# Optimization experiments

Hardware: AMD Instinct MI355X
Metric: run time of the kernel (lower is better)

## Reference

```python
import jax, jax.numpy as jnp
import numpy as np

B, N, D = 8, 1024, 768
H = 3
DCAT = 2 * D          # 1536, input dim at layer 1
DK = DCAT // H        # 512
CONV_OUT = D - 2      # 766 (kernel 3, VALID)


def setup_inputs() -> dict:
    key = jax.random.key(0)
    ks = jax.random.split(key, 20)
    s = 0.02
    return {
        "adj": jax.random.uniform(ks[0], (B, N, N), dtype=jnp.float32),
        "inputs": jax.random.normal(ks[1], (B, N, D), dtype=jnp.float32),
        "score_mask": jax.random.randint(ks[2], (B, H, N, N), 0, 2).astype(bool),
        # GCN layer weights (stored [in,out]; math = torch Linear)
        "W0_w": jax.random.normal(ks[3], (D, D), dtype=jnp.float32) * s,
        "W0_b": jnp.zeros((D,), dtype=jnp.float32),
        "W1_w": jax.random.normal(ks[4], (DCAT, D), dtype=jnp.float32) * s,
        "W1_b": jnp.zeros((D,), dtype=jnp.float32),
        # MultiHeadAttention(3, 1536) query/key projections
        "q_w": jax.random.normal(ks[5], (DCAT, DCAT), dtype=jnp.float32) * s,
        "q_b": jnp.zeros((DCAT,), dtype=jnp.float32),
        "k_w": jax.random.normal(ks[6], (DCAT, DCAT), dtype=jnp.float32) * s,
        "k_b": jnp.zeros((DCAT,), dtype=jnp.float32),
        # Conv1d(n, n, 3) created in forward: OIH layout
        "conv_w": jax.random.normal(ks[7], (N, N, 3), dtype=jnp.float32) * s,
        "conv_b": jnp.zeros((N,), dtype=jnp.float32),
        # linearc: 766 -> 768
        "linc_w": jax.random.normal(ks[8], (CONV_OUT, D), dtype=jnp.float32) * s,
        "linc_b": jnp.zeros((D,), dtype=jnp.float32),
        # fc: Linear(768,768,no bias) -> ReLU -> Linear(768,768,no bias)
        "fc1_w": jax.random.normal(ks[9], (D, D), dtype=jnp.float32) * s,
        "fc2_w": jax.random.normal(ks[10], (D, D), dtype=jnp.float32) * s,
    }


def _gcn_layer(adj, x, denom, Ww, Wb):
    Ax = adj @ x                       # [B,n,din]
    AxW = (Ax @ Ww + Wb) / denom       # [B,n,768]
    return jax.nn.relu(AxW) + (x @ Ww + Wb)


def _select_top2(m):
    # per-batch top-2 threshold over flattened NxN, symmetrize, diag=1
    b, n, _ = m.shape
    flat = m.reshape(b, -1)
    thr = jax.lax.top_k(flat, 2)[0][:, -1]                  # [b]
    mask = (flat >= thr[:, None]).astype(m.dtype).reshape(b, n, n)
    mask = mask + jnp.swapaxes(mask, -1, -2)
    eye = jnp.eye(n, dtype=m.dtype)
    return mask * (1.0 - eye) + eye


def reference(adj, inputs, score_mask, W0_w, W0_b, W1_w, W1_b,
              q_w, q_b, k_w, k_b, conv_w, conv_b, linc_w, linc_b,
              fc1_w, fc2_w):
    b, n, d = inputs.shape
    # ---- layer 0 ----
    denom = adj.sum(2, keepdims=True) + 1.0
    out = _gcn_layer(adj, inputs, denom, W0_w, W0_b)        # [B,n,768]
    # Conv1d over feature axis with channels = n, VALID, k=3 -> [B,n,766]
    conve = jax.nn.relu(
        jax.lax.conv_general_dilated(out, conv_w, (1,), 'VALID',
                                     dimension_numbers=('NCH', 'OIH', 'NCH'))
        + conv_b[None, :, None])
    out = conve @ linc_w + linc_b                           # [B,n,768]
    # ---- layer 1 (semantic path) ----
    x = jnp.concatenate([inputs, out], axis=-1)             # [B,n,1536]
    h, dk = H, x.shape[-1] // H
    q = (x @ q_w + q_b).reshape(b, n, h, dk).transpose(0, 2, 1, 3)
    k = (x @ k_w + k_b).reshape(b, n, h, dk).transpose(0, 2, 1, 3)
    scores = jnp.einsum('bhqd,bhkd->bhqk', q, k) / jnp.sqrt(jnp.float32(dk))
    scores = jnp.where(score_mask, jnp.float32(-1e9), scores)
    keep = (~score_mask[:, :, :, 0:1]).astype(scores.dtype)
    attn = jax.nn.softmax(scores, axis=-1) * keep           # [B,3,n,n]
    # attention-driven head selection (softmax over batch dim, argmax over heads)
    prob = jax.nn.softmax(attn.sum((-2, -1)), axis=0)       # [B,3]
    max_idx = jnp.argmax(prob, axis=1)                      # [B]
    adj2 = jnp.take_along_axis(attn, max_idx[:, None, None, None], axis=1)[:, 0]
    adj2 = _select_top2(adj2) * adj2
    denom2 = adj2.sum(2, keepdims=True) + 1.0
    out = _gcn_layer(adj2, x, denom2, W1_w, W1_b)
    out = jax.nn.relu(out @ fc1_w) @ fc2_w
    return out
```

## Files before the change

kernel.cpp:

```cpp
#include <hip/hip_runtime.h>
#include <cstdint>
#include <cstddef>

typedef __bf16 bf16;
typedef __bf16 bf16x8 __attribute__((ext_vector_type(8)));
typedef float f32x4 __attribute__((ext_vector_type(4)));

#define B_ 8
#define N_ 1024
#define D_ 768
#define H_ 3
#define DC_ 1536
#define DK_ 512
#define PC_ 766
#define MB_ (1024ull*1024ull)

static const size_t O_DEN   = 0;
static const size_t O_DEN2  = 32768;
static const size_t O_ADIAG = 65536;
static const size_t O_T2P   = 98304;
static const size_t O_THR   = 163840;
static const size_t O_CNTS  = 164096;
static const size_t O_HSEL  = 164352;
static const size_t O_SELC  = 164608;
static const size_t O_FLAG  = 164864;
static const size_t O_QKB   = 165120;
static const size_t O_SEL   = 180224;
static const size_t O_ATTN  = 262144;
static const size_t O_X     = O_ATTN + 32*MB_;
static const size_t O_AX2   = O_X    + 24*MB_;
static const size_t O_ADJB  = O_AX2  + 24*MB_;
static const size_t O_INT   = O_ADJB + 16*MB_;
static const size_t O_BBA   = O_INT  + 12*MB_;
static const size_t O_BBB   = O_BBA  + 12*MB_;
static const size_t O_BBC   = O_BBB  + 12*MB_;
static const size_t O_W0T   = O_BBC  + 12*MB_;
static const size_t O_W1T   = O_W0T + 1179648;
static const size_t O_QKWT  = O_W1T + 2359296;
static const size_t O_CWB   = O_QKWT + 9437184;
static const size_t O_LCT   = O_CWB + 6291456;
static const size_t O_F1T   = O_LCT + 1179648;
static const size_t O_F2T   = O_F1T + 1179648;
static const size_t WS_NEED = O_F2T + 1179648;
static const size_t O_OUT0T = O_INT;

__device__ __forceinline__ bool mask_at(const void* p, int flag, size_t i) {
    switch (flag) {
        case 1:  return ((const int*)p)[i] != 0;
        case 2:  return ((const float*)p)[i] != 0.0f;
        case 3:  return ((const long long*)p)[i] != 0;
        default: return ((const unsigned char*)p)[i] != 0;
    }
}

__device__ __forceinline__ void gload16(const void* g, void* l) {
    __builtin_amdgcn_global_load_lds(
        (const __attribute__((address_space(1))) void*)g,
        (__attribute__((address_space(3))) void*)l, 16, 0, 0);
}

__device__ inline float blockMax256(float v) {
    __shared__ float red[4];
    for (int off = 32; off; off >>= 1) v = fmaxf(v, __shfl_xor(v, off));
    int lane = threadIdx.x & 63, wid = threadIdx.x >> 6;
    if (lane == 0) red[wid] = v;
    __syncthreads();
    v = fmaxf(fmaxf(red[0], red[1]), fmaxf(red[2], red[3]));
    __syncthreads();
    return v;
}

__device__ inline float blockSum256(float v) {
    __shared__ float red[4];
    for (int off = 32; off; off >>= 1) v += __shfl_xor(v, off);
    int lane = threadIdx.x & 63, wid = threadIdx.x >> 6;
    if (lane == 0) red[wid] = v;
    __syncthreads();
    v = red[0] + red[1] + red[2] + red[3];
    __syncthreads();
    return v;
}

template<int EPI>
__global__ __launch_bounds__(256) void mm(
    const bf16* __restrict__ A, size_t sA, int lda,
    const bf16* __restrict__ Bt, size_t sB, int ldb,
    const int* __restrict__ rowIdx, int rowMul,
    const float* __restrict__ bias,
    const bf16* __restrict__ Dadd, int ldd,
    const float* __restrict__ denv,
    const void* __restrict__ smask, const int* __restrict__ flagp,
    bf16* __restrict__ Cb, float* __restrict__ Cf, size_t sC, int ldc,
    int M, int N, int K)
{
    __shared__ __align__(16) bf16 As[2][64 * 64];
    __shared__ __align__(16) bf16 Bs[2][128 * 64];

    const int gx = gridDim.x, gy = gridDim.y;
    const int nwg = gx * gy * (int)gridDim.z;
    int lin = ((int)blockIdx.z * gy + (int)blockIdx.y) * gx + (int)blockIdx.x;
    int cpx = nwg >> 3;
    int swz = (lin & 7) * cpx + (lin >> 3);
    int ty = swz % gy;
    int tt = swz / gy;
    int tx = tt % gx;
    int b  = tt / gx;

    const int bm = ty * 64, bn = tx * 128;
    const int tid = threadIdx.x;
    const int lane = tid & 63, w = tid >> 6;
    const int wr = w >> 1, wc = w & 1;
    const int boff = rowIdx ? rowIdx[b] * rowMul : 0;

    const bf16* Ab = A + (size_t)b * sA;
    const bf16* Bb = Bt + (size_t)b * sB;

    const int sr = lane >> 3;
    const int gk = ((lane & 7) ^ (lane >> 3)) * 8;

    f32x4 zero = {0.f, 0.f, 0.f, 0.f};
    f32x4 acc[2][4];
    #pragma unroll
    for (int i = 0; i < 2; ++i)
        #pragma unroll
        for (int j = 0; j < 4; ++j) acc[i][j] = zero;

    #pragma unroll
    for (int q = 0; q < 2; ++q)
        gload16((const void*)(Ab + (size_t)(bm + w * 16 + q * 8 + sr) * lda + gk),
                (void*)(As[0] + (w * 16 + q * 8) * 64));
    #pragma unroll
    for (int q = 0; q < 4; ++q)
        gload16((const void*)(Bb + (size_t)(boff + bn + w * 32 + q * 8 + sr) * ldb + gk),
                (void*)(Bs[0] + (w * 32 + q * 8) * 64));

    const int rl = lane & 15;
    const int g8 = lane >> 4;
    const int rx = lane & 7;

    int cur = 0;
    for (int k0 = 0; k0 < K; k0 += 64) {
        int nxt = cur ^ 1;
        if (k0 + 64 < K) {
            #pragma unroll
            for (int q = 0; q < 2; ++q)
                gload16((const void*)(Ab + (size_t)(bm + w * 16 + q * 8 + sr) * lda + k0 + 64 + gk),
                        (void*)(As[nxt] + (w * 16 + q * 8) * 64));
            #pragma unroll
            for (int q = 0; q < 4; ++q)
                gload16((const void*)(Bb + (size_t)(boff + bn + w * 32 + q * 8 + sr) * ldb + k0 + 64 + gk),
                        (void*)(Bs[nxt] + (w * 32 + q * 8) * 64));
            asm volatile("s_waitcnt vmcnt(6)" ::: "memory");
        } else {
            asm volatile("s_waitcnt vmcnt(0)" ::: "memory");
        }
        __builtin_amdgcn_s_barrier();
        __builtin_amdgcn_sched_barrier(0);

        bf16x8 af[2][2], bfv[4][2];
        #pragma unroll
        for (int ks = 0; ks < 2; ++ks) {
            int e = ks * 4 + g8;
            #pragma unroll
            for (int i = 0; i < 2; ++i)
                af[i][ks] = *(const bf16x8*)(As[cur] + (wr * 32 + i * 16 + rl) * 64 + (e ^ rx) * 8);
            #pragma unroll
            for (int j = 0; j < 4; ++j)
                bfv[j][ks] = *(const bf16x8*)(Bs[cur] + (wc * 64 + j * 16 + rl) * 64 + (e ^ rx) * 8);
        }
        #pragma unroll
        for (int ks = 0; ks < 2; ++ks)
            #pragma unroll
            for (int i = 0; i < 2; ++i)
                #pragma unroll
                for (int j = 0; j < 4; ++j)
                    acc[i][j] = __builtin_amdgcn_mfma_f32_16x16x32_bf16(af[i][ks], bfv[j][ks], acc[i][j], 0, 0, 0);

        __builtin_amdgcn_s_barrier();
        __builtin_amdgcn_sched_barrier(0);
        cur = nxt;
    }

    const int r0 = (lane >> 4) * 4, c0 = lane & 15;
    int flag = 0, h0 = 0;
    if (EPI == 4) { flag = flagp[0]; h0 = rowIdx[b]; }
    #pragma unroll
    for (int i = 0; i < 2; ++i) {
        #pragma unroll
        for (int r = 0; r < 4; ++r) {
            int m = bm + wr * 32 + i * 16 + r0 + r;
            #pragma unroll
            for (int j = 0; j < 4; ++j) {
                int n = bn + wc * 64 + j * 16 + c0;
                float v = acc[i][j][r];
                size_t oidx = (size_t)b * sC + (size_t)m * ldc + n;
                if (EPI == 0) {
                    Cb[oidx] = (bf16)(v + bias[boff + n]);
                } else if (EPI == 1) {
                    v = fmaxf((v + bias[n]) / denv[(size_t)b * M + m], 0.f)
                        + (float)Dadd[((size_t)b * M + m) * ldd + n];
                    Cb[oidx] = (bf16)v;
                } else if (EPI == 2) {
                    Cb[oidx] = (bf16)fmaxf(v, 0.f);
                } else if (EPI == 3) {
                    Cf[oidx] = v;
                } else if (EPI == 4) {
                    size_t mi = (((size_t)b * H_ + h0) * N_ + m) * N_ + n;
                    Cf[oidx] = mask_at(smask, flag, mi) ? -1e9f : v * 0.04419417382415922f;
                } else if (EPI == 5) {
                    Cb[oidx] = (n < PC_) ? (bf16)fmaxf(v + bias[m], 0.f) : (bf16)0.f;
                } else {
                    Cb[oidx] = (bf16)v;
                }
            }
        }
    }
}


__global__ __launch_bounds__(256) void k_detect(const unsigned int* __restrict__ sm,
                                                int* __restrict__ flag) {
    __shared__ int sGt1, sF32, sOddNZ;
    if (threadIdx.x == 0) { sGt1 = 0; sF32 = 0; sOddNZ = 0; }
    __syncthreads();
    int gt1 = 0, f32c = 0, oddnz = 0;
    for (int s = 0; s < 16; ++s) {
        int idx = s * 256 + threadIdx.x;
        unsigned wv = sm[idx];
        if (wv > 1u) gt1 = 1;
        if (wv == 0x3F800000u) f32c++;
        if ((idx & 1) && wv != 0u) oddnz = 1;
    }
    if (gt1)   atomicOr(&sGt1, 1);
    if (f32c)  atomicAdd(&sF32, f32c);
    if (oddnz) atomicOr(&sOddNZ, 1);
    __syncthreads();
    if (threadIdx.x == 0) {
        int f;
        if (sF32 > 512) f = 2;
        else if (!sGt1) f = sOddNZ ? 1 : 3;
        else f = 0;
        flag[0] = f;
    }
}

__global__ __launch_bounds__(256) void k_cvt_adj(const float* __restrict__ adj,
                                                 bf16* __restrict__ adjb,
                                                 float* __restrict__ den) {
    int b = blockIdx.y, row = blockIdx.x;
    size_t base = ((size_t)b * N_ + row) * N_;
    float4 v = ((const float4*)(adj + base))[threadIdx.x];
    union { bf16 b[4]; uint2 u; } o;
    o.b[0] = (bf16)v.x; o.b[1] = (bf16)v.y; o.b[2] = (bf16)v.z; o.b[3] = (bf16)v.w;
    ((uint2*)(adjb + base))[threadIdx.x] = o.u;
    float s = blockSum256(v.x + v.y + v.z + v.w);
    if (threadIdx.x == 0) den[b * N_ + row] = s + 1.0f;
}

__global__ __launch_bounds__(256) void k_cvtrows(const float* __restrict__ s,
                                                 bf16* __restrict__ d) {
    int row = blockIdx.x, t = threadIdx.x;
    if (t >= 192) return;
    float4 v = ((const float4*)(s + (size_t)row * D_))[t];
    union { bf16 b[4]; uint2 u; } o;
    o.b[0] = (bf16)v.x; o.b[1] = (bf16)v.y; o.b[2] = (bf16)v.z; o.b[3] = (bf16)v.w;
    *(uint2*)(d + (size_t)row * DC_ + t * 4) = o.u;
}

__global__ __launch_bounds__(256) void k_cw2(const float* __restrict__ w,
                                             bf16* __restrict__ d) {
    int o = blockIdx.x;
    const float* s = w + (size_t)o * 3072;
    bf16* dp = d + (size_t)o * 3072;
    for (int q = 0; q < 4; ++q) {
        int i = q * 256 + threadIdx.x;
        float v0 = s[i * 3], v1 = s[i * 3 + 1], v2 = s[i * 3 + 2];
        dp[i] = (bf16)v0; dp[1024 + i] = (bf16)v1; dp[2048 + i] = (bf16)v2;
    }
}

__global__ __launch_bounds__(256) void k_qkb(const float* __restrict__ qb,
                                             const float* __restrict__ kb,
                                             float* __restrict__ d) {
    int idx = blockIdx.x * 256 + threadIdx.x;
    if (idx >= 3072) return;
    int h = idx >> 10, rem = idx & 1023, s = rem >> 9, r = rem & 511;
    d[idx] = (s ? kb : qb)[h * 512 + r];
}

__global__ __launch_bounds__(256) void k_trcvt(
    const float* __restrict__ src, bf16* __restrict__ dst,
    int R, int C, int Rpad, int Cpad, size_t sSrc, size_t sDst, int mode)
{
    __shared__ float t[32][33];
    int b = blockIdx.z;
    int r0 = blockIdx.y * 32, c0 = blockIdx.x * 32;
    int tx = threadIdx.x & 31, ty = threadIdx.x >> 5;
    const float* s = src + (size_t)b * sSrc;
    bf16* d = dst + (size_t)b * sDst;
    #pragma unroll
    for (int q = 0; q < 4; ++q) {
        int r = r0 + ty + q * 8, c = c0 + tx;
        t[ty + q * 8][tx] = (r < R && c < C) ? s[(size_t)r * C + c] : 0.f;
    }
    __syncthreads();
    #pragma unroll
    for (int q = 0; q < 4; ++q) {
        int dr = c0 + ty + q * 8, dc = r0 + tx;
        if (dr < Cpad && dc < Rpad) {
            int drm = dr;
            if (mode == 1) drm = (dr >> 9) * 1024 + (dr & 511);
            else if (mode == 2) drm = (dr >> 9) * 1024 + 512 + (dr & 511);
            d[(size_t)drm * Rpad + dc] = (bf16)t[tx][ty + q * 8];
        }
    }
}

__global__ __launch_bounds__(256) void k_tr_bf16(const bf16* __restrict__ src,
                                                 bf16* __restrict__ dst) {
    __shared__ bf16 t[32][34];
    int b = blockIdx.z;
    int i0 = blockIdx.y * 32, p0 = blockIdx.x * 32;
    int tx = threadIdx.x & 31, ty = threadIdx.x >> 5;
    const bf16* s = src + (size_t)b * N_ * D_;
    bf16* d = dst + (size_t)b * D_ * N_;
    #pragma unroll
    for (int q = 0; q < 4; ++q)
        t[ty + q * 8][tx] = s[(size_t)(i0 + ty + q * 8) * D_ + p0 + tx];
    __syncthreads();
    #pragma unroll
    for (int q = 0; q < 4; ++q)
        d[(size_t)(p0 + ty + q * 8) * N_ + i0 + tx] = t[tx][ty + q * 8];
}

__global__ __launch_bounds__(256) void k_softmax(float* __restrict__ Sc,
                                                 const void* __restrict__ smask,
                                                 const int* __restrict__ flagp,
                                                 const int* __restrict__ hsel,
                                                 float* __restrict__ part) {
    __shared__ float s1[256], s2[256];
    int b = blockIdx.y, row = blockIdx.x;
    int h0 = hsel[b], flag = flagp[0];
    float* rp = Sc + ((size_t)b * N_ + row) * N_;
    float v[4];
    float mx = -INFINITY;
    #pragma unroll
    for (int s = 0; s < 4; ++s) { v[s] = rp[s * 256 + threadIdx.x]; mx = fmaxf(mx, v[s]); }
    mx = blockMax256(mx);
    float sum = 0.f;
    #pragma unroll
    for (int s = 0; s < 4; ++s) { v[s] = expf(v[s] - mx); sum += v[s]; }
    sum = blockSum256(sum);
    size_t ki = (((size_t)b * H_ + h0) * N_ + row) * N_;
    float keep = mask_at(smask, flag, ki) ? 0.f : 1.f;
    float inv = keep / sum;
    float m1 = -INFINITY, m2 = -INFINITY;
    #pragma unroll
    for (int s = 0; s < 4; ++s) {
        float x = v[s] * inv;
        rp[s * 256 + threadIdx.x] = x;
        if (x > m1) { m2 = m1; m1 = x; } else m2 = fmaxf(m2, x);
    }
    int tid = threadIdx.x;
    s1[tid] = m1; s2[tid] = m2;
    __syncthreads();
    for (int off = 128; off; off >>= 1) {
        if (tid < off) {
            float a1 = s1[tid], a2 = s2[tid], b1 = s1[tid + off], b2 = s2[tid + off];
            s1[tid] = fmaxf(a1, b1);
            s2[tid] = fmaxf(fminf(a1, b1), fmaxf(a2, b2));
        }
        __syncthreads();
    }
    if (tid == 0) {
        part[((size_t)b * N_ + row) * 2]     = s1[0];
        part[((size_t)b * N_ + row) * 2 + 1] = s2[0];
    }
}

__global__ __launch_bounds__(256) void k_count(const void* __restrict__ smask,
                                               const int* __restrict__ flagp,
                                               int* __restrict__ counts) {
    int bh = blockIdx.x, flag = flagp[0];
    float c = 0.f;
    for (int s = 0; s < 4; ++s) {
        int q = s * 256 + threadIdx.x;
        size_t mi = ((size_t)bh * N_ + q) * N_;
        if (!mask_at(smask, flag, mi)) c += 1.f;
    }
    c = blockSum256(c);
    if (threadIdx.x == 0) counts[bh] = (int)(c + 0.5f);
}

__global__ void k_select_head(const int* __restrict__ counts, int* __restrict__ hsel) {
    if (threadIdx.x != 0 || blockIdx.x != 0) return;
    float p[B_][H_];
    for (int h = 0; h < H_; ++h) {
        float mx = -1e30f;
        for (int b = 0; b < B_; ++b) mx = fmaxf(mx, (float)counts[b * H_ + h]);
        float s = 0.f;
        for (int b = 0; b < B_; ++b) { p[b][h] = expf((float)counts[b * H_ + h] - mx); s += p[b][h]; }
        for (int b = 0; b < B_; ++b) p[b][h] /= s;
    }
    for (int b = 0; b < B_; ++b) {
        int best = 0; float bv = p[b][0];
        for (int h = 1; h < H_; ++h) if (p[b][h] > bv) { bv = p[b][h]; best = h; }
        hsel[b] = best;
    }
}

__global__ __launch_bounds__(256) void k_top2_s2(const float* __restrict__ part,
                                                 float* __restrict__ thr,
                                                 int* __restrict__ selcnt) {
    __shared__ float s1[256], s2[256];
    int b = blockIdx.x, tid = threadIdx.x;
    float m1 = -INFINITY, m2 = -INFINITY;
    for (int s = 0; s < 4; ++s) {
        int r = s * 256 + tid;
        float a1 = part[((size_t)b * N_ + r) * 2];
        float a2 = part[((size_t)b * N_ + r) * 2 + 1];
        float n1 = fmaxf(m1, a1);
        float n2 = fmaxf(fminf(m1, a1), fmaxf(m2, a2));
        m1 = n1; m2 = n2;
    }
    s1[tid] = m1; s2[tid] = m2;
    __syncthreads();
    for (int off = 128; off; off >>= 1) {
        if (tid < off) {
            float a1 = s1[tid], a2 = s2[tid], b1 = s1[tid + off], b2 = s2[tid + off];
            s1[tid] = fmaxf(a1, b1);
            s2[tid] = fmaxf(fminf(a1, b1), fmaxf(a2, b2));
        }
        __syncthreads();
    }
    if (tid == 0) { thr[b] = s2[0]; selcnt[b] = 0; }
}

__global__ __launch_bounds__(256) void k_extract(const float* __restrict__ attn,
                                                 const float* __restrict__ thr,
                                                 int* __restrict__ selcnt,
                                                 int* __restrict__ sel,
                                                 float* __restrict__ adiag,
                                                 float* __restrict__ den2) {
    int b = blockIdx.y, row = blockIdx.x;
    const float* ap = attn + (size_t)b * N_ * N_;
    float t = thr[b];
    size_t base = (size_t)row * 1024;
    for (int s = 0; s < 4; ++s) {
        int col = s * 256 + threadIdx.x;
        float v = ap[base + col];
        if (col == row) {
            adiag[b * N_ + row] = v;
            den2[b * N_ + row] = v + 1.0f;
        }
        if (v >= t) {
            int pos = atomicAdd(&selcnt[b], 1);
            if (pos < 512) {
                sel[((size_t)b * 512 + pos) * 2]     = row;
                sel[((size_t)b * 512 + pos) * 2 + 1] = col;
            }
        }
    }
}

__global__ __launch_bounds__(256) void k_ax2_init(const bf16* __restrict__ x,
                                                  const float* __restrict__ adiag,
                                                  bf16* __restrict__ ax2) {
    int row = blockIdx.x;
    float a = adiag[row];
    const bf16* xp = x + (size_t)row * DC_;
    bf16* op = ax2 + (size_t)row * DC_;
    for (int s = 0; s < 6; ++s) {
        int d = s * 256 + threadIdx.x;
        op[d] = (bf16)(a * (float)xp[d]);
    }
}

__global__ __launch_bounds__(256) void k_ax2_sparse(const float* __restrict__ attn,
                                                    const bf16* __restrict__ x,
                                                    const int* __restrict__ selcnt,
                                                    const int* __restrict__ sel,
                                                    bf16* __restrict__ ax2,
                                                    float* __restrict__ den2) {
    int b = blockIdx.x;
    int cnt = selcnt[b]; if (cnt > 512) cnt = 512;
    __shared__ int si[1024];
    if (threadIdx.x == 0) {
        for (int e = 0; e < cnt; ++e) {
            si[e * 2]     = sel[((size_t)b * 512 + e) * 2];
            si[e * 2 + 1] = sel[((size_t)b * 512 + e) * 2 + 1];
        }
        for (int a = 1; a < cnt; ++a) {
            int ii = si[a * 2], jj = si[a * 2 + 1];
            long long key = (long long)ii * N_ + jj;
            int p = a - 1;
            while (p >= 0 && ((long long)si[p * 2] * N_ + si[p * 2 + 1]) > key) {
                si[(p + 1) * 2] = si[p * 2]; si[(p + 1) * 2 + 1] = si[p * 2 + 1]; --p;
            }
            si[(p + 1) * 2] = ii; si[(p + 1) * 2 + 1] = jj;
        }
    }
    __syncthreads();
    const float* ap = attn + (size_t)b * N_ * N_;
    for (int e = 0; e < cnt; ++e) {
        int i = si[e * 2], j = si[e * 2 + 1];
        if (i == j) continue;
        float aij = ap[(size_t)i * N_ + j];
        float aji = ap[(size_t)j * N_ + i];
        bf16* ri = ax2 + ((size_t)b * N_ + i) * DC_;
        bf16* rj = ax2 + ((size_t)b * N_ + j) * DC_;
        const bf16* xi = x + ((size_t)b * N_ + i) * DC_;
        const bf16* xj = x + ((size_t)b * N_ + j) * DC_;
        for (int s = 0; s < 6; ++s) {
            int d = s * 256 + threadIdx.x;
            ri[d] = (bf16)((float)ri[d] + aij * (float)xj[d]);
            rj[d] = (bf16)((float)rj[d] + aji * (float)xi[d]);
        }
        if (threadIdx.x == 0) {
            den2[b * N_ + i] += aij;
            den2[b * N_ + j] += aji;
        }
        __syncthreads();
    }
}

extern "C" void kernel_launch(void* const* d_in, const int* in_sizes, int n_in,
                              void* d_out, int out_size, void* d_ws, size_t ws_size,
                              hipStream_t stream) {
    if (n_in < 17) return;
    if (ws_size < WS_NEED) return;

    const float* adj    = (const float*)d_in[0];
    const float* inputs = (const float*)d_in[1];
    const void*  smask  = d_in[2];
    const float* W0w = (const float*)d_in[3];
    const float* W0b = (const float*)d_in[4];
    const float* W1w = (const float*)d_in[5];
    const float* W1b = (const float*)d_in[6];
    const float* qw  = (const float*)d_in[7];
    const float* qb  = (const float*)d_in[8];
    const float* kw  = (const float*)d_in[9];
    const float* kb  = (const float*)d_in[10];
    const float* convw = (const float*)d_in[11];
    const float* convb = (const float*)d_in[12];
    const float* lincw = (const float*)d_in[13];
    const float* lincb = (const float*)d_in[14];
    const float* fc1w  = (const float*)d_in[15];
    const float* fc2w  = (const float*)d_in[16];

    char* W = (char*)d_ws;
    float* out = (float*)d_out;

    float* den    = (float*)(W + O_DEN);
    float* den2   = (float*)(W + O_DEN2);
    float* adiag  = (float*)(W + O_ADIAG);
    float* t2p    = (float*)(W + O_T2P);
    float* thr    = (float*)(W + O_THR);
    int*   counts = (int*)(W + O_CNTS);
    int*   hsel   = (int*)(W + O_HSEL);
    int*   selcnt = (int*)(W + O_SELC);
    int*   flag   = (int*)(W + O_FLAG);
    float* qkb    = (float*)(W + O_QKB);
    int*   sel    = (int*)(W + O_SEL);
    float* ATTN   = (float*)(W + O_ATTN);
    bf16* X     = (bf16*)(W + O_X);
    bf16* AX2   = (bf16*)(W + O_AX2);
    bf16* QKOUT = (bf16*)(W + O_AX2);
    bf16* ADJB  = (bf16*)(W + O_ADJB);
    bf16* INT_  = (bf16*)(W + O_INT);
    bf16* OUT0T = (bf16*)(W + O_OUT0T);
    bf16* BBA   = (bf16*)(W + O_BBA);
    bf16* BBB   = (bf16*)(W + O_BBB);
    bf16* BBC   = (bf16*)(W + O_BBC);
    bf16* W0T   = (bf16*)(W + O_W0T);
    bf16* W1T   = (bf16*)(W + O_W1T);
    bf16* QKWT  = (bf16*)(W + O_QKWT);
    bf16* CW2   = (bf16*)(W + O_CWB);
    bf16* LCT   = (bf16*)(W + O_LCT);
    bf16* F1T   = (bf16*)(W + O_F1T);
    bf16* F2T   = (bf16*)(W + O_F2T);

    const size_t sND  = (size_t)N_ * D_;
    const size_t sNDC = (size_t)N_ * DC_;
    const size_t sNN  = (size_t)N_ * N_;

    k_detect<<<1, 256, 0, stream>>>((const unsigned int*)smask, flag);
    k_cvt_adj<<<dim3(N_, B_), 256, 0, stream>>>(adj, ADJB, den);
    k_cvtrows<<<B_ * N_, 256, 0, stream>>>(inputs, X);
    k_cw2<<<1024, 256, 0, stream>>>(convw, CW2);
    k_qkb<<<12, 256, 0, stream>>>(qb, kb, qkb);
    k_trcvt<<<dim3(24, 32, B_), 256, 0, stream>>>(inputs, INT_, N_, D_, N_, D_, sND, sND, 0);
    k_trcvt<<<dim3(24, 24, 1), 256, 0, stream>>>(W0w, W0T, D_, D_, D_, D_, 0, 0, 0);
    k_trcvt<<<dim3(24, 48, 1), 256, 0, stream>>>(W1w, W1T, DC_, D_, DC_, D_, 0, 0, 0);
    k_trcvt<<<dim3(48, 48, 1), 256, 0, stream>>>(qw, QKWT, DC_, DC_, DC_, DC_, 0, 0, 1);
    k_trcvt<<<dim3(48, 48, 1), 256, 0, stream>>>(kw, QKWT, DC_, DC_, DC_, DC_, 0, 0, 2);
    k_trcvt<<<dim3(24, 24, 1), 256, 0, stream>>>(lincw, LCT, PC_, D_, D_, D_, 0, 0, 0);
    k_trcvt<<<dim3(24, 24, 1), 256, 0, stream>>>(fc1w, F1T, D_, D_, D_, D_, 0, 0, 0);
    k_trcvt<<<dim3(24, 24, 1), 256, 0, stream>>>(fc2w, F2T, D_, D_, D_, D_, 0, 0, 0);

    mm<0><<<dim3(6, 16, B_), 256, 0, stream>>>(X, sNDC, DC_, W0T, 0, D_, nullptr, 0,
        W0b, nullptr, 0, nullptr, nullptr, nullptr, BBA, nullptr, sND, D_, N_, D_, D_);
    mm<6><<<dim3(6, 16, B_), 256, 0, stream>>>(ADJB, sNN, N_, INT_, sND, N_, nullptr, 0,
        nullptr, nullptr, 0, nullptr, nullptr, nullptr, BBB, nullptr, sND, D_, N_, D_, N_);
    mm<1><<<dim3(6, 16, B_), 256, 0, stream>>>(BBB, sND, D_, W0T, 0, D_, nullptr, 0,
        W0b, BBA, D_, den, nullptr, nullptr, BBC, nullptr, sND, D_, N_, D_, D_);
    k_tr_bf16<<<dim3(24, 32, B_), 256, 0, stream>>>(BBC, OUT0T);
    mm<5><<<dim3(6, 16, B_), 256, 0, stream>>>(CW2, 0, 3072, OUT0T, sND, N_, nullptr, 0,
        convb, nullptr, 0, nullptr, nullptr, nullptr, BBB, nullptr, sND, D_, N_, D_, 3072);
    mm<0><<<dim3(6, 16, B_), 256, 0, stream>>>(BBB, sND, D_, LCT, 0, D_, nullptr, 0,
        lincb, nullptr, 0, nullptr, nullptr, nullptr, X + D_, nullptr, sNDC, DC_, N_, D_, D_);

    k_count<<<B_ * H_, 256, 0, stream>>>(smask, flag, counts);
    k_select_head<<<1, 64, 0, stream>>>(counts, hsel);

    mm<0><<<dim3(8, 16, B_), 256, 0, stream>>>(X, sNDC, DC_, QKWT, 0, DC_, hsel, 1024,
        qkb, nullptr, 0, nullptr, nullptr, nullptr, QKOUT, nullptr, sNN, N_, N_, N_, DC_);
    mm<4><<<dim3(8, 16, B_), 256, 0, stream>>>(QKOUT, sNN, N_, QKOUT + 512, sNN, N_, hsel, 0,
        nullptr, nullptr, 0, nullptr, smask, flag, nullptr, ATTN, sNN, N_, N_, N_, DK_);
    k_softmax<<<dim3(N_, B_), 256, 0, stream>>>(ATTN, smask, flag, hsel, t2p);

    k_top2_s2<<<B_, 256, 0, stream>>>(t2p, thr, selcnt);
    k_extract<<<dim3(N_, B_), 256, 0, stream>>>(ATTN, thr, selcnt, sel, adiag, den2);
    k_ax2_init<<<B_ * N_, 256, 0, stream>>>(X, adiag, AX2);
    k_ax2_sparse<<<B_, 256, 0, stream>>>(ATTN, X, selcnt, sel, AX2, den2);

    mm<0><<<dim3(6, 16, B_), 256, 0, stream>>>(X, sNDC, DC_, W1T, 0, DC_, nullptr, 0,
        W1b, nullptr, 0, nullptr, nullptr, nullptr, BBA, nullptr, sND, D_, N_, D_, DC_);
    mm<1><<<dim3(6, 16, B_), 256, 0, stream>>>(AX2, sNDC, DC_, W1T, 0, DC_, nullptr, 0,
        W1b, BBA, D_, den2, nullptr, nullptr, BBB, nullptr, sND, D_, N_, D_, DC_);

    mm<2><<<dim3(6, 16, B_), 256, 0, stream>>>(BBB, sND, D_, F1T, 0, D_, nullptr, 0,
        nullptr, nullptr, 0, nullptr, nullptr, nullptr, BBC, nullptr, sND, D_, N_, D_, D_);
    mm<3><<<dim3(6, 16, B_), 256, 0, stream>>>(BBC, sND, D_, F2T, 0, D_, nullptr, 0,
        nullptr, nullptr, 0, nullptr, nullptr, nullptr, nullptr, out, sND, D_, N_, D_, D_);
}
```

Baseline: 436.8 us.

## Merge prep kernels into one launch and fuse QK with W1 projection GEMM

Collapses the many small preprocessing launches (detect, conversions, transposes, mask counts) into one block-dispatched prep kernel. It also computes the x@W1 GEMM inside the Q/K projection launch by widening its grid to 1792 output columns, and folds the diagonal AX2 init into k_extract. The aim is to cut launch overhead and let small kernels fill the GPU together. The mask-count blocks each redo the detection step locally, and the merged GEMM writes to two outputs through a new epilogue.

```diff
diff --git a/kernel.cpp b/kernel.cpp
--- a/kernel.cpp
+++ b/kernel.cpp
@@ -91,7 +91,9 @@
     const float* __restrict__ denv,
     const void* __restrict__ smask, const int* __restrict__ flagp,
     bf16* __restrict__ Cb, float* __restrict__ Cf, size_t sC, int ldc,
-    int M, int N, int K)
+    int M, int N, int K,
+    const bf16* __restrict__ Bt2, const float* __restrict__ bias2,
+    bf16* __restrict__ Cb2, size_t sC2, int ldc2)
 {
     __shared__ __align__(16) bf16 As[2][64 * 64];
     __shared__ __align__(16) bf16 Bs[2][128 * 64];
@@ -115,6 +117,10 @@
     const bf16* Ab = A + (size_t)b * sA;
     const bf16* Bb = Bt + (size_t)b * sB;
 
+    const bf16* Bsrc = Bb;
+    int bRow0 = boff + bn;
+    if (EPI == 7 && bn >= 1024) { Bsrc = Bt2; bRow0 = bn - 1024; }
+
     const int sr = lane >> 3;
     const int gk = ((lane & 7) ^ (lane >> 3)) * 8;
 
@@ -131,7 +137,7 @@
                 (void*)(As[0] + (w * 16 + q * 8) * 64));
     #pragma unroll
     for (int q = 0; q < 4; ++q)
-        gload16((const void*)(Bb + (size_t)(boff + bn + w * 32 + q * 8 + sr) * ldb + gk),
+        gload16((const void*)(Bsrc + (size_t)(bRow0 + w * 32 + q * 8 + sr) * ldb + gk),
                 (void*)(Bs[0] + (w * 32 + q * 8) * 64));
 
     const int rl = lane & 15;
@@ -148,7 +154,7 @@
                         (void*)(As[nxt] + (w * 16 + q * 8) * 64));
             #pragma unroll
             for (int q = 0; q < 4; ++q)
-                gload16((const void*)(Bb + (size_t)(boff + bn + w * 32 + q * 8 + sr) * ldb + k0 + 64 + gk),
+                gload16((const void*)(Bsrc + (size_t)(bRow0 + w * 32 + q * 8 + sr) * ldb + k0 + 64 + gk),
                         (void*)(Bs[nxt] + (w * 32 + q * 8) * 64));
             asm volatile("s_waitcnt vmcnt(6)" ::: "memory");
         } else {
@@ -209,6 +215,11 @@
                     Cf[oidx] = mask_at(smask, flag, mi) ? -1e9f : v * 0.04419417382415922f;
                 } else if (EPI == 5) {
                     Cb[oidx] = (n < PC_) ? (bf16)fmaxf(v + bias[m], 0.f) : (bf16)0.f;
+                } else if (EPI == 7) {
+                    if (n < 1024)
+                        Cb[(size_t)b * sC + (size_t)m * ldc + n] = (bf16)(v + bias[boff + n]);
+                    else
+                        Cb2[(size_t)b * sC2 + (size_t)m * ldc2 + (n - 1024)] = (bf16)(v + bias2[n - 1024]);
                 } else {
                     Cb[oidx] = (bf16)v;
                 }
@@ -218,9 +229,8 @@
 }
 
 
-__global__ __launch_bounds__(256) void k_detect(const unsigned int* __restrict__ sm,
-                                                int* __restrict__ flag) {
-    __shared__ int sGt1, sF32, sOddNZ;
+__device__ int d_detect(const unsigned int* __restrict__ sm) {
+    __shared__ int sGt1, sF32, sOddNZ, sFlag;
     if (threadIdx.x == 0) { sGt1 = 0; sF32 = 0; sOddNZ = 0; }
     __syncthreads();
     int gt1 = 0, f32c = 0, oddnz = 0;
@@ -240,64 +250,20 @@
         if (sF32 > 512) f = 2;
         else if (!sGt1) f = sOddNZ ? 1 : 3;
         else f = 0;
-        flag[0] = f;
-    }
-}
-
-__global__ __launch_bounds__(256) void k_cvt_adj(const float* __restrict__ adj,
-                                                 bf16* __restrict__ adjb,
-                                                 float* __restrict__ den) {
-    int b = blockIdx.y, row = blockIdx.x;
-    size_t base = ((size_t)b * N_ + row) * N_;
-    float4 v = ((const float4*)(adj + base))[threadIdx.x];
-    union { bf16 b[4]; uint2 u; } o;
-    o.b[0] = (bf16)v.x; o.b[1] = (bf16)v.y; o.b[2] = (bf16)v.z; o.b[3] = (bf16)v.w;
-    ((uint2*)(adjb + base))[threadIdx.x] = o.u;
-    float s = blockSum256(v.x + v.y + v.z + v.w);
-    if (threadIdx.x == 0) den[b * N_ + row] = s + 1.0f;
-}
-
-__global__ __launch_bounds__(256) void k_cvtrows(const float* __restrict__ s,
-                                                 bf16* __restrict__ d) {
-    int row = blockIdx.x, t = threadIdx.x;
-    if (t >= 192) return;
-    float4 v = ((const float4*)(s + (size_t)row * D_))[t];
-    union { bf16 b[4]; uint2 u; } o;
-    o.b[0] = (bf16)v.x; o.b[1] = (bf16)v.y; o.b[2] = (bf16)v.z; o.b[3] = (bf16)v.w;
-    *(uint2*)(d + (size_t)row * DC_ + t * 4) = o.u;
-}
-
-__global__ __launch_bounds__(256) void k_cw2(const float* __restrict__ w,
-                                             bf16* __restrict__ d) {
-    int o = blockIdx.x;
-    const float* s = w + (size_t)o * 3072;
-    bf16* dp = d + (size_t)o * 3072;
-    for (int q = 0; q < 4; ++q) {
-        int i = q * 256 + threadIdx.x;
-        float v0 = s[i * 3], v1 = s[i * 3 + 1], v2 = s[i * 3 + 2];
-        dp[i] = (bf16)v0; dp[1024 + i] = (bf16)v1; dp[2048 + i] = (bf16)v2;
-    }
-}
-
-__global__ __launch_bounds__(256) void k_qkb(const float* __restrict__ qb,
-                                             const float* __restrict__ kb,
-                                             float* __restrict__ d) {
-    int idx = blockIdx.x * 256 + threadIdx.x;
-    if (idx >= 3072) return;
-    int h = idx >> 10, rem = idx & 1023, s = rem >> 9, r = rem & 511;
-    d[idx] = (s ? kb : qb)[h * 512 + r];
-}
-
-__global__ __launch_bounds__(256) void k_trcvt(
-    const float* __restrict__ src, bf16* __restrict__ dst,
-    int R, int C, int Rpad, int Cpad, size_t sSrc, size_t sDst, int mode)
-{
+        sFlag = f;
+    }
+    __syncthreads();
+    return sFlag;
+}
+
+__device__ void d_trcvt(const float* __restrict__ src, bf16* __restrict__ dst,
+                        int R, int C, int Rpad, int Cpad,
+                        size_t sSrc, size_t sDst, int mode, int bx, int by, int bz) {
     __shared__ float t[32][33];
-    int b = blockIdx.z;
-    int r0 = blockIdx.y * 32, c0 = blockIdx.x * 32;
+    int r0 = by * 32, c0 = bx * 32;
     int tx = threadIdx.x & 31, ty = threadIdx.x >> 5;
-    const float* s = src + (size_t)b * sSrc;
-    bf16* d = dst + (size_t)b * sDst;
+    const float* s = src + (size_t)bz * sSrc;
+    bf16* d = dst + (size_t)bz * sDst;
     #pragma unroll
     for (int q = 0; q < 4; ++q) {
         int r = r0 + ty + q * 8, c = c0 + tx;
@@ -313,6 +279,130 @@
             else if (mode == 2) drm = (dr >> 9) * 1024 + 512 + (dr & 511);
             d[(size_t)drm * Rpad + dc] = (bf16)t[tx][ty + q * 8];
         }
+    }
+}
+
+#define PB_DET   1
+#define PB_QKB   13
+#define PB_CW2   1037
+#define PB_ADJ   9229
+#define PB_ROWS  17421
+#define PB_INT   23565
+#define PB_W0    24141
+#define PB_W1    25293
+#define PB_QW    27597
+#define PB_KW    29901
+#define PB_LC    30477
+#define PB_F1    31053
+#define PB_F2    31629
+#define PB_CNT   31653
+
+__global__ __launch_bounds__(256) void k_prep(
+    const void* __restrict__ smask, int* __restrict__ flag, int* __restrict__ counts,
+    const float* __restrict__ adj, bf16* __restrict__ adjb, float* __restrict__ den,
+    const float* __restrict__ inputs, bf16* __restrict__ X, bf16* __restrict__ INT_,
+    const float* __restrict__ convw, bf16* __restrict__ CW2,
+    const float* __restrict__ qb, const float* __restrict__ kb, float* __restrict__ qkbD,
+    const float* __restrict__ W0w, bf16* __restrict__ W0T,
+    const float* __restrict__ W1w, bf16* __restrict__ W1T,
+    const float* __restrict__ qw, const float* __restrict__ kw, bf16* __restrict__ QKWT,
+    const float* __restrict__ lincw, bf16* __restrict__ LCT,
+    const float* __restrict__ fc1w, bf16* __restrict__ F1T,
+    const float* __restrict__ fc2w, bf16* __restrict__ F2T)
+{
+    const int id = blockIdx.x;
+    const size_t sND = (size_t)N_ * D_;
+    if (id < PB_DET) {
+        int f = d_detect((const unsigned int*)smask);
+        if (threadIdx.x == 0) flag[0] = f;
+    } else if (id < PB_QKB) {
+        int idx = (id - PB_DET) * 256 + threadIdx.x;
+        if (idx < 3072) {
+            int h = idx >> 10, rem = idx & 1023, s = rem >> 9, r = rem & 511;
+            qkbD[idx] = (s ? kb : qb)[h * 512 + r];
+        }
+    } else if (id < PB_CW2) {
+        int o = id - PB_QKB;
+        const float* s = convw + (size_t)o * 3072;
+        bf16* dp = CW2 + (size_t)o * 3072;
+        for (int q = 0; q < 4; ++q) {
+            int i = q * 256 + threadIdx.x;
+            float v0 = s[i * 3], v1 = s[i * 3 + 1], v2 = s[i * 3 + 2];
+            dp[i] = (bf16)v0; dp[1024 + i] = (bf16)v1; dp[2048 + i] = (bf16)v2;
+        }
+    } else if (id < PB_ADJ) {
+        int t = id - PB_CW2;
+        int row = t & 1023, b = t >> 10;
+        size_t base = ((size_t)b * N_ + row) * N_;
+        float4 v = ((const float4*)(adj + base))[threadIdx.x];
+        union { bf16 b[4]; uint2 u; } o;
+        o.b[0] = (bf16)v.x; o.b[1] = (bf16)v.y; o.b[2] = (bf16)v.z; o.b[3] = (bf16)v.w;
+        ((uint2*)(adjb + base))[threadIdx.x] = o.u;
+        float s = blockSum256(v.x + v.y + v.z + v.w);
+        if (threadIdx.x == 0) den[b * N_ + row] = s + 1.0f;
+    } else if (id < PB_ROWS) {
+        int row = id - PB_ADJ;
+        int t = threadIdx.x;
+        if (t < 192) {
+            float4 v = ((const float4*)(inputs + (size_t)row * D_))[t];
+            union { bf16 b[4]; uint2 u; } o;
+            o.b[0] = (bf16)v.x; o.b[1] = (bf16)v.y; o.b[2] = (bf16)v.z; o.b[3] = (bf16)v.w;
+            *(uint2*)(X + (size_t)row * DC_ + t * 4) = o.u;
+        }
+    } else if (id < PB_INT) {
+        int t = id - PB_ROWS;
+        int bx = t % 24; int u = t / 24; int by = u % 32; int bz = u / 32;
+        d_trcvt(inputs, INT_, N_, D_, N_, D_, sND, sND, 0, bx, by, bz);
+    } else if (id < PB_W0) {
+        int t = id - PB_INT;
+        d_trcvt(W0w, W0T, D_, D_, D_, D_, 0, 0, 0, t % 24, t / 24, 0);
+    } else if (id < PB_W1) {
+        int t = id - PB_W0;
+        d_trcvt(W1w, W1T, DC_, D_, DC_, D_, 0, 0, 0, t % 24, t / 24, 0);
+    } else if (id < PB_QW) {
+        int t = id - PB_W1;
+        d_trcvt(qw, QKWT, DC_, DC_, DC_, DC_, 0, 0, 1, t % 48, t / 48, 0);
+    } else if (id < PB_KW) {
+        int t = id - PB_QW;
+        d_trcvt(kw, QKWT, DC_, DC_, DC_, DC_, 0, 0, 2, t % 48, t / 48, 0);
+    } else if (id < PB_LC) {
+        int t = id - PB_KW;
+        d_trcvt(lincw, LCT, PC_, D_, D_, D_, 0, 0, 0, t % 24, t / 24, 0);
+    } else if (id < PB_F1) {
+        int t = id - PB_LC;
+        d_trcvt(fc1w, F1T, D_, D_, D_, D_, 0, 0, 0, t % 24, t / 24, 0);
+    } else if (id < PB_F2) {
+        int t = id - PB_F1;
+        d_trcvt(fc2w, F2T, D_, D_, D_, D_, 0, 0, 0, t % 24, t / 24, 0);
+    } else if (id < PB_CNT) {
+        int bh = id - PB_F2;
+        int f = d_detect((const unsigned int*)smask);
+        float c = 0.f;
+        for (int s = 0; s < 4; ++s) {
+            int q = s * 256 + threadIdx.x;
+            size_t mi = ((size_t)bh * N_ + q) * N_;
+            if (!mask_at(smask, f, mi)) c += 1.f;
+        }
+        c = blockSum256(c);
+        if (threadIdx.x == 0) counts[bh] = (int)(c + 0.5f);
+    }
+}
+
+
+__global__ void k_select_head(const int* __restrict__ counts, int* __restrict__ hsel) {
+    if (threadIdx.x != 0 || blockIdx.x != 0) return;
+    float p[B_][H_];
+    for (int h = 0; h < H_; ++h) {
+        float mx = -1e30f;
+        for (int b = 0; b < B_; ++b) mx = fmaxf(mx, (float)counts[b * H_ + h]);
+        float s = 0.f;
+        for (int b = 0; b < B_; ++b) { p[b][h] = expf((float)counts[b * H_ + h] - mx); s += p[b][h]; }
+        for (int b = 0; b < B_; ++b) p[b][h] /= s;
+    }
+    for (int b = 0; b < B_; ++b) {
+        int best = 0; float bv = p[b][0];
+        for (int h = 1; h < H_; ++h) if (p[b][h] > bv) { bv = p[b][h]; best = h; }
+        hsel[b] = best;
     }
 }
 
@@ -375,37 +465,6 @@
     if (tid == 0) {
         part[((size_t)b * N_ + row) * 2]     = s1[0];
         part[((size_t)b * N_ + row) * 2 + 1] = s2[0];
-    }
-}
-
-__global__ __launch_bounds__(256) void k_count(const void* __restrict__ smask,
-                                               const int* __restrict__ flagp,
-                                               int* __restrict__ counts) {
-    int bh = blockIdx.x, flag = flagp[0];
-    float c = 0.f;
-    for (int s = 0; s < 4; ++s) {
-        int q = s * 256 + threadIdx.x;
-        size_t mi = ((size_t)bh * N_ + q) * N_;
-        if (!mask_at(smask, flag, mi)) c += 1.f;
-    }
-    c = blockSum256(c);
-    if (threadIdx.x == 0) counts[bh] = (int)(c + 0.5f);
-}
-
-__global__ void k_select_head(const int* __restrict__ counts, int* __restrict__ hsel) {
-    if (threadIdx.x != 0 || blockIdx.x != 0) return;
-    float p[B_][H_];
-    for (int h = 0; h < H_; ++h) {
-        float mx = -1e30f;
-        for (int b = 0; b < B_; ++b) mx = fmaxf(mx, (float)counts[b * H_ + h]);
-        float s = 0.f;
-        for (int b = 0; b < B_; ++b) { p[b][h] = expf((float)counts[b * H_ + h] - mx); s += p[b][h]; }
-        for (int b = 0; b < B_; ++b) p[b][h] /= s;
-    }
-    for (int b = 0; b < B_; ++b) {
-        int best = 0; float bv = p[b][0];
-        for (int h = 1; h < H_; ++h) if (p[b][h] > bv) { bv = p[b][h]; best = h; }
-        hsel[b] = best;
     }
 }
 
@@ -441,7 +500,10 @@
                                                  int* __restrict__ selcnt,
                                                  int* __restrict__ sel,
                                                  float* __restrict__ adiag,
-                                                 float* __restrict__ den2) {
+                                                 float* __restrict__ den2,
+                                                 const bf16* __restrict__ x,
+                                                 bf16* __restrict__ ax2) {
+    __shared__ float sdiag;
     int b = blockIdx.y, row = blockIdx.x;
     const float* ap = attn + (size_t)b * N_ * N_;
     float t = thr[b];
@@ -452,6 +514,7 @@
         if (col == row) {
             adiag[b * N_ + row] = v;
             den2[b * N_ + row] = v + 1.0f;
+            sdiag = v;
         }
         if (v >= t) {
             int pos = atomicAdd(&selcnt[b], 1);
@@ -461,15 +524,11 @@
             }
         }
     }
-}
-
-__global__ __launch_bounds__(256) void k_ax2_init(const bf16* __restrict__ x,
-                                                  const float* __restrict__ adiag,
-                                                  bf16* __restrict__ ax2) {
-    int row = blockIdx.x;
-    float a = adiag[row];
-    const bf16* xp = x + (size_t)row * DC_;
-    bf16* op = ax2 + (size_t)row * DC_;
+    __syncthreads();
+    float a = sdiag;
+    const bf16* xp = x + ((size_t)b * N_ + row) * DC_;
+    bf16* op = ax2 + ((size_t)b * N_ + row) * DC_;
+    #pragma unroll
     for (int s = 0; s < 6; ++s) {
         int d = s * 256 + threadIdx.x;
         op[d] = (bf16)(a * (float)xp[d]);
@@ -584,53 +643,50 @@
     const size_t sNDC = (size_t)N_ * DC_;
     const size_t sNN  = (size_t)N_ * N_;
 
-    k_detect<<<1, 256, 0, stream>>>((const unsigned int*)smask, flag);
-    k_cvt_adj<<<dim3(N_, B_), 256, 0, stream>>>(adj, ADJB, den);
-    k_cvtrows<<<B_ * N_, 256, 0, stream>>>(inputs, X);
-    k_cw2<<<1024, 256, 0, stream>>>(convw, CW2);
-    k_qkb<<<12, 256, 0, stream>>>(qb, kb, qkb);
-    k_trcvt<<<dim3(24, 32, B_), 256, 0, stream>>>(inputs, INT_, N_, D_, N_, D_, sND, sND, 0);
-    k_trcvt<<<dim3(24, 24, 1), 256, 0, stream>>>(W0w, W0T, D_, D_, D_, D_, 0, 0, 0);
-    k_trcvt<<<dim3(24, 48, 1), 256, 0, stream>>>(W1w, W1T, DC_, D_, DC_, D_, 0, 0, 0);
-    k_trcvt<<<dim3(48, 48, 1), 256, 0, stream>>>(qw, QKWT, DC_, DC_, DC_, DC_, 0, 0, 1);
-    k_trcvt<<<dim3(48, 48, 1), 256, 0, stream>>>(kw, QKWT, DC_, DC_, DC_, DC_, 0, 0, 2);
-    k_trcvt<<<dim3(24, 24, 1), 256, 0, stream>>>(lincw, LCT, PC_, D_, D_, D_, 0, 0, 0);
-    k_trcvt<<<dim3(24, 24, 1), 256, 0, stream>>>(fc1w, F1T, D_, D_, D_, D_, 0, 0, 0);
-    k_trcvt<<<dim3(24, 24, 1), 256, 0, stream>>>(fc2w, F2T, D_, D_, D_, D_, 0, 0, 0);
+    k_prep<<<PB_CNT, 256, 0, stream>>>(smask, flag, counts,
+        adj, ADJB, den, inputs, X, INT_, convw, CW2,
+        qb, kb, qkb, W0w, W0T, W1w, W1T, qw, kw, QKWT,
+        lincw, LCT, fc1w, F1T, fc2w, F2T);
+    k_select_head<<<1, 64, 0, stream>>>(counts, hsel);
 
     mm<0><<<dim3(6, 16, B_), 256, 0, stream>>>(X, sNDC, DC_, W0T, 0, D_, nullptr, 0,
-        W0b, nullptr, 0, nullptr, nullptr, nullptr, BBA, nullptr, sND, D_, N_, D_, D_);
+        W0b, nullptr, 0, nullptr, nullptr, nullptr, BBA, nullptr, sND, D_, N_, D_, D_,
+        nullptr, nullptr, nullptr, 0, 0);
     mm<6><<<dim3(6, 16, B_), 256, 0, stream>>>(ADJB, sNN, N_, INT_, sND, N_, nullptr, 0,
-        nullptr, nullptr, 0, nullptr, nullptr, nullptr, BBB, nullptr, sND, D_, N_, D_, N_);
+        nullptr, nullptr, 0, nullptr, nullptr, nullptr, BBB, nullptr, sND, D_, N_, D_, N_,
+        nullptr, nullptr, nullptr, 0, 0);
     mm<1><<<dim3(6, 16, B_), 256, 0, stream>>>(BBB, sND, D_, W0T, 0, D_, nullptr, 0,
-        W0b, BBA, D_, den, nullptr, nullptr, BBC, nullptr, sND, D_, N_, D_, D_);
+        W0b, BBA, D_, den, nullptr, nullptr, BBC, nullptr, sND, D_, N_, D_, D_,
+        nullptr, nullptr, nullptr, 0, 0);
     k_tr_bf16<<<dim3(24, 32, B_), 256, 0, stream>>>(BBC, OUT0T);
     mm<5><<<dim3(6, 16, B_), 256, 0, stream>>>(CW2, 0, 3072, OUT0T, sND, N_, nullptr, 0,
-        convb, nullptr, 0, nullptr, nullptr, nullptr, BBB, nullptr, sND, D_, N_, D_, 3072);
+        convb, nullptr, 0, nullptr, nullptr, nullptr, BBB, nullptr, sND, D_, N_, D_, 3072,
+        nullptr, nullptr, nullptr, 0, 0);
     mm<0><<<dim3(6, 16, B_), 256, 0, stream>>>(BBB, sND, D_, LCT, 0, D_, nullptr, 0,
-        lincb, nullptr, 0, nullptr, nullptr, nullptr, X + D_, nullptr, sNDC, DC_, N_, D_, D_);
-
-    k_count<<<B_ * H_, 256, 0, stream>>>(smask, flag, counts);
-    k_select_head<<<1, 64, 0, stream>>>(counts, hsel);
-
-    mm<0><<<dim3(8, 16, B_), 256, 0, stream>>>(X, sNDC, DC_, QKWT, 0, DC_, hsel, 1024,
-        qkb, nullptr, 0, nullptr, nullptr, nullptr, QKOUT, nullptr, sNN, N_, N_, N_, DC_);
+        lincb, nullptr, 0, nullptr, nullptr, nullptr, X + D_, nullptr, sNDC, DC_, N_, D_, D_,
+        nullptr, nullptr, nullptr, 0, 0);
+
+    mm<7><<<dim3(14, 16, B_), 256, 0, stream>>>(X, sNDC, DC_, QKWT, 0, DC_, hsel, 1024,
+        qkb, nullptr, 0, nullptr, nullptr, nullptr, QKOUT, nullptr, sNN, N_, N_, 1792, DC_,
+        W1T, W1b, BBA, sND, D_);
+
     mm<4><<<dim3(8, 16, B_), 256, 0, stream>>>(QKOUT, sNN, N_, QKOUT + 512, sNN, N_, hsel, 0,
-        nullptr, nullptr, 0, nullptr, smask, flag, nullptr, ATTN, sNN, N_, N_, N_, DK_);
+        nullptr, nullptr, 0, nullptr, smask, flag, nullptr, ATTN, sNN, N_, N_, N_, DK_,
+        nullptr, nullptr, nullptr, 0, 0);
     k_softmax<<<dim3(N_, B_), 256, 0, stream>>>(ATTN, smask, flag, hsel, t2p);
 
     k_top2_s2<<<B_, 256, 0, stream>>>(t2p, thr, selcnt);
-    k_extract<<<dim3(N_, B_), 256, 0, stream>>>(ATTN, thr, selcnt, sel, adiag, den2);
-    k_ax2_init<<<B_ * N_, 256, 0, stream>>>(X, adiag, AX2);
+    k_extract<<<dim3(N_, B_), 256, 0, stream>>>(ATTN, thr, selcnt, sel, adiag, den2, X, AX2);
     k_ax2_sparse<<<B_, 256, 0, stream>>>(ATTN, X, selcnt, sel, AX2, den2);
 
-    mm<0><<<dim3(6, 16, B_), 256, 0, stream>>>(X, sNDC, DC_, W1T, 0, DC_, nullptr, 0,
-        W1b, nullptr, 0, nullptr, nullptr, nullptr, BBA, nullptr, sND, D_, N_, D_, DC_);
     mm<1><<<dim3(6, 16, B_), 256, 0, stream>>>(AX2, sNDC, DC_, W1T, 0, DC_, nullptr, 0,
-        W1b, BBA, D_, den2, nullptr, nullptr, BBB, nullptr, sND, D_, N_, D_, DC_);
+        W1b, BBA, D_, den2, nullptr, nullptr, BBB, nullptr, sND, D_, N_, D_, DC_,
+        nullptr, nullptr, nullptr, 0, 0);
 
     mm<2><<<dim3(6, 16, B_), 256, 0, stream>>>(BBB, sND, D_, F1T, 0, D_, nullptr, 0,
-        nullptr, nullptr, 0, nullptr, nullptr, nullptr, BBC, nullptr, sND, D_, N_, D_, D_);
+        nullptr, nullptr, 0, nullptr, nullptr, nullptr, BBC, nullptr, sND, D_, N_, D_, D_,
+        nullptr, nullptr, nullptr, 0, 0);
     mm<3><<<dim3(6, 16, B_), 256, 0, stream>>>(BBC, sND, D_, F2T, 0, D_, nullptr, 0,
-        nullptr, nullptr, 0, nullptr, nullptr, nullptr, nullptr, out, sND, D_, N_, D_, D_);
-}
+        nullptr, nullptr, 0, nullptr, nullptr, nullptr, nullptr, out, sND, D_, N_, D_, D_,
+        nullptr, nullptr, nullptr, 0, 0);
+}
```

Measured after the change: 407.0 us, median of 2. -6.8%, faster.
